# Kernel optimization log

Measured on AMD Instinct MI355X. Metric: run time of the kernel, lower is better.

## Reference

```python
import jax, jax.numpy as jnp
import numpy as np

K = 32  # num_nearest_neighbors

def silu(x):
    return x * jax.nn.sigmoid(x)

def setup_inputs() -> dict:
    key = jax.random.key(0)
    ks = jax.random.split(key, 10)
    b, n, d, m = 4, 2048, 64, 16
    e_in = 2 * d + 1  # 129 = fourier*2 + dim*2 + edge_dim + 1
    std = 0.001  # init_eps normal init on Linear weights
    inp = {
        "feats": jax.random.normal(ks[0], (b, n, d), dtype=jnp.float32),
        "coors": jax.random.normal(ks[1], (b, n, 3), dtype=jnp.float32),
        # edge_mlp: Linear(129,258) -> SiLU -> Linear(258,16) -> SiLU
        "ew1": jax.random.normal(ks[2], (e_in, 2 * e_in), dtype=jnp.float32) * std,
        "eb1": jnp.zeros((2 * e_in,), dtype=jnp.float32),
        "ew2": jax.random.normal(ks[3], (2 * e_in, m), dtype=jnp.float32) * std,
        "eb2": jnp.zeros((m,), dtype=jnp.float32),
        # coors_mlp: Linear(16,64) -> SiLU -> Linear(64,1)
        "cw1": jax.random.normal(ks[4], (m, 4 * m), dtype=jnp.float32) * std,
        "cb1": jnp.zeros((4 * m,), dtype=jnp.float32),
        "cw2": jax.random.normal(ks[5], (4 * m, 1), dtype=jnp.float32) * std,
        "cb2": jnp.zeros((1,), dtype=jnp.float32),
        # node_mlp: Linear(80,128) -> SiLU -> Linear(128,64)
        "nw1": jax.random.normal(ks[6], (d + m, 2 * d), dtype=jnp.float32) * std,
        "nb1": jnp.zeros((2 * d,), dtype=jnp.float32),
        "nw2": jax.random.normal(ks[7], (2 * d, d), dtype=jnp.float32) * std,
        "nb2": jnp.zeros((d,), dtype=jnp.float32),
    }
    return inp


def reference(feats, coors, ew1, eb1, ew2, eb2, cw1, cb1, cw2, cb2, nw1, nb1, nw2, nb2):
    b, n, d = feats.shape
    # pairwise relative coords / squared distances: [b,n,n,3], [b,n,n]
    rel = coors[:, :, None, :] - coors[:, None, :, :]
    dist2 = jnp.sum(rel * rel, axis=-1)
    # k nearest neighbors (smallest squared distance)
    _, idx = jax.lax.top_k(-dist2, K)  # idx: [b,n,K]
    bi = jnp.arange(b)[:, None, None]
    ii = jnp.arange(n)[None, :, None]
    rel_k = rel[bi, ii, idx]                # [b,n,K,3]
    dist_k = dist2[bi, ii, idx][..., None]  # [b,n,K,1]
    feats_j = feats[bi, idx]                # [b,n,K,d]
    feats_i = jnp.broadcast_to(feats[:, :, None, :], feats_j.shape)
    # edge MLP
    edge_in = jnp.concatenate([feats_i, feats_j, dist_k], axis=-1)  # [b,n,K,2d+1]
    h = silu(edge_in @ ew1 + eb1)
    m_ij = silu(h @ ew2 + eb2)  # [b,n,K,m]
    # coordinate update
    coor_w = (silu(m_ij @ cw1 + cb1) @ cw2 + cb2)[..., 0]  # [b,n,K]
    coors_out = jnp.einsum('bik,bikc->bic', coor_w, rel_k) + coors
    # node update (sum pooling over neighbors)
    m_i = jnp.sum(m_ij, axis=-2)  # [b,n,m]
    node_in = jnp.concatenate([feats, m_i], axis=-1)
    node_out = silu(node_in @ nw1 + nb1) @ nw2 + nb2 + feats
    return (node_out, coors_out)
```

## Files before the change

### kernel.cpp

```cpp
#include <hip/hip_runtime.h>
#include <math.h>

#define NB 4
#define NN 2048
#define ND 64
#define NM 16
#define NK 32
#define EIN 129
#define EH 258
#define CHD 64
#define NHD 128
#define PQS 288
#define KNN_BLOCKS (NB * NN / 4)
#define PREP_BLOCKS 90

typedef __attribute__((ext_vector_type(8))) short short8;
typedef __attribute__((ext_vector_type(4))) float f32x4;
typedef __attribute__((ext_vector_type(4))) int intx4;

__device__ __forceinline__ float fast_silu(float x) {
    return x * __builtin_amdgcn_rcpf(1.f + __expf(-x));
}

__device__ __forceinline__ short f2bf(float f) {
    union { float f; unsigned u; } v; v.f = f;
    unsigned r = v.u + 0x7FFFu + ((v.u >> 16) & 1u);
    return (short)(r >> 16);
}

__device__ __forceinline__ float bf2f(short s) {
    union { unsigned u; float f; } v;
    v.u = ((unsigned)(unsigned short)s) << 16;
    return v.f;
}

__device__ __forceinline__ unsigned cvt_pk_bf16(float lo, float hi) {
    unsigned r;
    asm("v_cvt_pk_bf16_f32 %0, %1, %2" : "=v"(r) : "v"(lo), "v"(hi));
    return r;
}

__device__ __forceinline__ unsigned umin_u(unsigned a, unsigned b) { return a < b ? a : b; }
__device__ __forceinline__ unsigned umax_u(unsigned a, unsigned b) { return a > b ? a : b; }

__global__ __launch_bounds__(256) void pk_kernel(
    const float* __restrict__ coors, int* __restrict__ idx_out,
    const float* __restrict__ ew1, const float* __restrict__ ew2, const float* __restrict__ eb1,
    const float* __restrict__ cw1,
    float* __restrict__ w1pad, float* __restrict__ eb1pad,
    short* __restrict__ W2T, short* __restrict__ W1F, short* __restrict__ cw1T) {
    __shared__ union {
        float clds[NN * 3];
        unsigned slds[4][NN];
    } sm;
    const int tid = threadIdx.x;

    if (blockIdx.x >= KNN_BLOCKS) {
        const int blk = blockIdx.x - KNN_BLOCKS;
        if (blk < 72) {
            const int kk = blk & 1, ct = (blk >> 1) % 18, half = blk / 36;
            for (int t = tid; t < 512; t += 256) {
                const int l = t >> 3, i = t & 7;
                const int er = l & 15, grp = l >> 4;
                const int k = kk * 32 + grp * 8 + i;
                const int col = ct * 16 + er;
                const int row = half * 64 + k;
                W1F[blk * 512 + t] = (col < EH) ? f2bf(ew1[row * EH + col]) : (short)0;
            }
        } else if (blk == 72) {
            for (int c = tid; c < PQS; c += 256) {
                w1pad[c] = (c < EH) ? ew1[128 * EH + c] : 0.f;
                eb1pad[c] = (c < EH) ? eb1[c] : 0.f;
            }
        } else if (blk < 89) {
            const int t = blk - 73;
            for (int k = tid; k < PQS; k += 256)
                W2T[t * PQS + k] = (k < EH) ? f2bf(ew2[k * NM + t]) : (short)0;
        } else {
            for (int t2 = tid; t2 < CHD * NM; t2 += 256) {
                const int h = t2 >> 4, t = t2 & 15;
                cw1T[t2] = f2bf(cw1[t * CHD + h]);
            }
        }
        return;
    }

    const int wv = tid >> 6;
    const int lane = tid & 63;
    const int row0 = blockIdx.x * 4;
    const int b = row0 >> 11;
    const float* cb = coors + (size_t)b * NN * 3;
    for (int t = tid; t < NN * 3; t += 256) sm.clds[t] = cb[t];
    __syncthreads();

    const int row = row0 + wv;
    const int i = row & (NN - 1);
    const float cix = sm.clds[i * 3 + 0], ciy = sm.clds[i * 3 + 1], ciz = sm.clds[i * 3 + 2];

    unsigned k[32];
    #pragma unroll
    for (int t = 0; t < 32; ++t) {
        int j = lane + 64 * t;
        float dx = cix - sm.clds[j * 3 + 0];
        float dy = ciy - sm.clds[j * 3 + 1];
        float dz = ciz - sm.clds[j * 3 + 2];
        float d = dx * dx + dy * dy + dz * dz;
        union { float f; unsigned u; } v; v.f = d;
        k[t] = (v.u & 0xFFFFF800u) | (unsigned)j;
    }
    __syncthreads();

    #pragma unroll
    for (int size = 2; size <= 32; size <<= 1) {
        #pragma unroll
        for (int stride = size >> 1; stride > 0; stride >>= 1) {
            #pragma unroll
            for (int t = 0; t < 32; ++t) {
                int p = t ^ stride;
                if (p > t) {
                    const bool up = ((t & size) == 0);
                    unsigned lo = umin_u(k[t], k[p]);
                    unsigned hi = umax_u(k[t], k[p]);
                    k[t] = up ? lo : hi;
                    k[p] = up ? hi : lo;
                }
            }
        }
    }
    #pragma unroll
    for (int t = 0; t < 32; ++t) sm.slds[wv][t * 64 + lane] = k[t];

    unsigned cur = k[0];
    int head = 0;
    int myidx = 0;
    for (int it = 0; it < NK; ++it) {
        unsigned w = cur;
        #pragma unroll
        for (int off = 1; off < 64; off <<= 1) {
            unsigned o = __shfl_xor(w, off);
            w = umin_u(w, o);
        }
        if (lane == it) myidx = (int)(w & 2047u);
        if (cur == w) {
            ++head;
            cur = (head < 32) ? sm.slds[wv][head * 64 + lane] : 0xFFFFFFFFu;
        }
    }
    if (lane < NK) idx_out[row * NK + lane] = myidx;
}

__global__ __launch_bounds__(256) void pq_kernel(const float* __restrict__ feats,
                                                 const short* __restrict__ W1F,
                                                 const float* __restrict__ eb1pad,
                                                 short* __restrict__ P,
                                                 short* __restrict__ Q) {
    const int wv = threadIdx.x >> 6, lane = threadIdx.x & 63;
    const int er = lane & 15, grp = lane >> 4;
    const int wid = blockIdx.x * 4 + wv;
    const int mt = wid / 18, ct = wid % 18;
    const int nb = mt * 16;

    short8 a[2];
    #pragma unroll
    for (int kk = 0; kk < 2; ++kk) {
        const float* fp = feats + (size_t)(nb + er) * ND + kk * 32 + grp * 8;
        f32x4 f0 = *(const f32x4*)fp;
        f32x4 f1 = *(const f32x4*)(fp + 4);
        union { intx4 iv; short8 s; } u;
        u.iv[0] = cvt_pk_bf16(f0[0], f0[1]);
        u.iv[1] = cvt_pk_bf16(f0[2], f0[3]);
        u.iv[2] = cvt_pk_bf16(f1[0], f1[1]);
        u.iv[3] = cvt_pk_bf16(f1[2], f1[3]);
        a[kk] = u.s;
    }

    const short8* WF = (const short8*)W1F;
    short8 bP0 = WF[((0 * 18 + ct) * 2 + 0) * 64 + lane];
    short8 bP1 = WF[((0 * 18 + ct) * 2 + 1) * 64 + lane];
    short8 bQ0 = WF[((1 * 18 + ct) * 2 + 0) * 64 + lane];
    short8 bQ1 = WF[((1 * 18 + ct) * 2 + 1) * 64 + lane];

    f32x4 accP = {0.f, 0.f, 0.f, 0.f};
    f32x4 accQ = {0.f, 0.f, 0.f, 0.f};
    accP = __builtin_amdgcn_mfma_f32_16x16x32_bf16(a[0], bP0, accP, 0, 0, 0);
    accP = __builtin_amdgcn_mfma_f32_16x16x32_bf16(a[1], bP1, accP, 0, 0, 0);
    accQ = __builtin_amdgcn_mfma_f32_16x16x32_bf16(a[0], bQ0, accQ, 0, 0, 0);
    accQ = __builtin_amdgcn_mfma_f32_16x16x32_bf16(a[1], bQ1, accQ, 0, 0, 0);

    const float bias = eb1pad[ct * 16 + er];
    #pragma unroll
    for (int r = 0; r < 4; ++r) {
        const int node = nb + grp * 4 + r;
        P[(size_t)node * PQS + ct * 16 + er] = f2bf(accP[r] + bias);
        Q[(size_t)node * PQS + ct * 16 + er] = f2bf(accQ[r]);
    }
}

__global__ __launch_bounds__(256) void edge_kernel(
    const float* __restrict__ coors, const int* __restrict__ idx,
    const short* __restrict__ P, const short* __restrict__ Q,
    const float* __restrict__ w1pad, const short* __restrict__ W2T,
    const float* __restrict__ eb2,
    const short* __restrict__ cw1T, const float* __restrict__ cb1,
    const float* __restrict__ cw2, const float* __restrict__ cb2,
    const float* __restrict__ feats,
    const float* __restrict__ nw1, const float* __restrict__ nb1,
    const float* __restrict__ nw2, const float* __restrict__ nb2,
    float* __restrict__ coors_out, float* __restrict__ node_out) {

    __shared__ __align__(16) short mtl[4][NK][NM];
    __shared__ float xs[4][80];
    __shared__ float hbuf[4][NHD];

    const int tid = threadIdx.x;
    const int wv = tid >> 6, lane = tid & 63;
    const int er = lane & 15, grp = lane >> 4;
    const int gi = blockIdx.x * 4 + wv;
    const int b = gi >> 11;

    xs[wv][lane] = feats[(size_t)gi * ND + lane];

    const int j0 = idx[gi * NK + er];
    const int j1 = idx[gi * NK + 16 + er];
    const float ci0 = coors[gi * 3 + 0], ci1 = coors[gi * 3 + 1], ci2 = coors[gi * 3 + 2];
    const float* cj0p = coors + (size_t)(b * NN + j0) * 3;
    const float* cj1p = coors + (size_t)(b * NN + j1) * 3;
    const float r0x = ci0 - cj0p[0], r0y = ci1 - cj0p[1], r0z = ci2 - cj0p[2];
    const float r1x = ci0 - cj1p[0], r1y = ci1 - cj1p[1], r1z = ci2 - cj1p[2];
    const float d0 = r0x * r0x + r0y * r0y + r0z * r0z;
    const float d1 = r1x * r1x + r1y * r1y + r1z * r1z;

    const short8* Pr8 = (const short8*)(P + (size_t)gi * PQS);
    const short8* Q0 = (const short8*)(Q + (size_t)(b * NN + j0) * PQS);
    const short8* Q1 = (const short8*)(Q + (size_t)(b * NN + j1) * PQS);
    const short8* w2row = (const short8*)(W2T + er * PQS);
    const f32x4* w14 = (const f32x4*)w1pad;

    f32x4 acc0 = {0.f, 0.f, 0.f, 0.f};
    f32x4 acc1 = {0.f, 0.f, 0.f, 0.f};
    #pragma unroll
    for (int kk = 0; kk < 9; ++kk) {
        short8 bf = w2row[kk * 4 + grp];
        short8 pb = Pr8[kk * 4 + grp];
        short8 qb0 = Q0[kk * 4 + grp];
        short8 qb1 = Q1[kk * 4 + grp];
        f32x4 w0 = w14[kk * 8 + grp * 2];
        f32x4 w1 = w14[kk * 8 + grp * 2 + 1];
        float wf[8] = {w0[0], w0[1], w0[2], w0[3], w1[0], w1[1], w1[2], w1[3]};
        float pf[8];
        #pragma unroll
        for (int i = 0; i < 8; ++i) pf[i] = bf2f(pb[i]);
        float h0[8], h1[8];
        #pragma unroll
        for (int i = 0; i < 8; ++i) {
            h0[i] = fast_silu(fmaf(d0, wf[i], pf[i]) + bf2f(qb0[i]));
            h1[i] = fast_silu(fmaf(d1, wf[i], pf[i]) + bf2f(qb1[i]));
        }
        union { intx4 iv; short8 s; } u0, u1;
        u0.iv[0] = cvt_pk_bf16(h0[0], h0[1]);
        u0.iv[1] = cvt_pk_bf16(h0[2], h0[3]);
        u0.iv[2] = cvt_pk_bf16(h0[4], h0[5]);
        u0.iv[3] = cvt_pk_bf16(h0[6], h0[7]);
        u1.iv[0] = cvt_pk_bf16(h1[0], h1[1]);
        u1.iv[1] = cvt_pk_bf16(h1[2], h1[3]);
        u1.iv[2] = cvt_pk_bf16(h1[4], h1[5]);
        u1.iv[3] = cvt_pk_bf16(h1[6], h1[7]);
        acc0 = __builtin_amdgcn_mfma_f32_16x16x32_bf16(u0.s, bf, acc0, 0, 0, 0);
        acc1 = __builtin_amdgcn_mfma_f32_16x16x32_bf16(u1.s, bf, acc1, 0, 0, 0);
    }

    const float eb2v = eb2[er];
    float m0[4], m1[4];
    #pragma unroll
    for (int r = 0; r < 4; ++r) {
        m0[r] = fast_silu(acc0[r] + eb2v);
        m1[r] = fast_silu(acc1[r] + eb2v);
    }

    float s = m0[0] + m0[1] + m0[2] + m0[3] + m1[0] + m1[1] + m1[2] + m1[3];
    s += __shfl_xor(s, 16);
    s += __shfl_xor(s, 32);
    if (lane < NM) xs[wv][ND + er] = s;

    #pragma unroll
    for (int r = 0; r < 4; ++r) {
        mtl[wv][grp * 4 + r][er] = f2bf(m0[r]);
        mtl[wv][16 + grp * 4 + r][er] = f2bf(m1[r]);
    }
    __syncthreads();

    const short8 zero8 = {0, 0, 0, 0, 0, 0, 0, 0};
    short8 afr[4];
    #pragma unroll
    for (int mt = 0; mt < 4; ++mt)
        afr[mt] = (grp < 2) ? *(const short8*)(cw1T + (mt * 16 + er) * NM + grp * 8) : zero8;

    float cwv[2];
    #pragma unroll
    for (int nt = 0; nt < 2; ++nt) {
        short8 bfr = (grp < 2) ? *(const short8*)&mtl[wv][nt * 16 + er][grp * 8] : zero8;
        float partial = 0.f;
        #pragma unroll
        for (int mt = 0; mt < 4; ++mt) {
            f32x4 dz = {0.f, 0.f, 0.f, 0.f};
            dz = __builtin_amdgcn_mfma_f32_16x16x32_bf16(afr[mt], bfr, dz, 0, 0, 0);
            f32x4 cb1v = *(const f32x4*)(cb1 + mt * 16 + grp * 4);
            f32x4 cw2v = *(const f32x4*)(cw2 + mt * 16 + grp * 4);
            #pragma unroll
            for (int r = 0; r < 4; ++r)
                partial += fast_silu(dz[r] + cb1v[r]) * cw2v[r];
        }
        partial += __shfl_xor(partial, 16);
        partial += __shfl_xor(partial, 32);
        cwv[nt] = partial + cb2[0];
    }

    float wx = cwv[0] * r0x + cwv[1] * r1x;
    float wy = cwv[0] * r0y + cwv[1] * r1y;
    float wz = cwv[0] * r0z + cwv[1] * r1z;
    #pragma unroll
    for (int off = 1; off < 16; off <<= 1) {
        wx += __shfl_xor(wx, off);
        wy += __shfl_xor(wy, off);
        wz += __shfl_xor(wz, off);
    }
    if (lane == 0) {
        coors_out[gi * 3 + 0] = ci0 + wx;
        coors_out[gi * 3 + 1] = ci1 + wy;
        coors_out[gi * 3 + 2] = ci2 + wz;
    }

    float a0 = nb1[lane], a1 = nb1[64 + lane];
    #pragma unroll 4
    for (int k = 0; k < 80; ++k) {
        float x = xs[wv][k];
        a0 += x * nw1[(size_t)k * NHD + lane];
        a1 += x * nw1[(size_t)k * NHD + 64 + lane];
    }
    hbuf[wv][lane] = fast_silu(a0);
    hbuf[wv][64 + lane] = fast_silu(a1);
    __syncthreads();

    float o = nb2[lane];
    #pragma unroll 4
    for (int k = 0; k < NHD; ++k) o += hbuf[wv][k] * nw2[(size_t)k * ND + lane];
    node_out[(size_t)gi * ND + lane] = o + xs[wv][lane];
}

extern "C" void kernel_launch(void* const* d_in, const int* in_sizes, int n_in,
                              void* d_out, int out_size, void* d_ws, size_t ws_size,
                              hipStream_t stream) {
    const float* feats = (const float*)d_in[0];
    const float* coors = (const float*)d_in[1];
    const float* ew1 = (const float*)d_in[2];
    const float* eb1 = (const float*)d_in[3];
    const float* ew2 = (const float*)d_in[4];
    const float* eb2 = (const float*)d_in[5];
    const float* cw1 = (const float*)d_in[6];
    const float* cb1 = (const float*)d_in[7];
    const float* cw2 = (const float*)d_in[8];
    const float* cb2 = (const float*)d_in[9];
    const float* nw1 = (const float*)d_in[10];
    const float* nb1 = (const float*)d_in[11];
    const float* nw2 = (const float*)d_in[12];
    const float* nb2 = (const float*)d_in[13];

    float* out_node = (float*)d_out;
    float* out_coors = out_node + (size_t)NB * NN * ND;

    char* ws = (char*)d_ws;
    int*   idx    = (int*)(ws + 0);
    short* P      = (short*)(ws + 1048576);
    short* Q      = (short*)(ws + 5767168);
    float* w1pad  = (float*)(ws + 10485760);
    float* eb1pad = (float*)(ws + 10486912);
    short* W2T    = (short*)(ws + 10488064);
    short* W1F    = (short*)(ws + 10497280);
    short* cw1T   = (short*)(ws + 10571008);

    pk_kernel<<<KNN_BLOCKS + PREP_BLOCKS, 256, 0, stream>>>(
        coors, idx, ew1, ew2, eb1, cw1, w1pad, eb1pad, W2T, W1F, cw1T);
    pq_kernel<<<(512 * 18) / 4, 256, 0, stream>>>(feats, W1F, eb1pad, P, Q);
    edge_kernel<<<NB * NN / 4, 256, 0, stream>>>(
        coors, idx, P, Q, w1pad, W2T, eb2, cw1T, cb1, cw2, cb2,
        feats, nw1, nb1, nw2, nb2, out_coors, out_node);
}
```

Before: 103.8 us.

## Move node MLP into separate MFMA kernel with bf16 staged inputs

Splits the node update out of the edge kernel into a new node_kernel that runs both node MLP layers with bf16 MFMA on 16-node tiles. Its input is staged through a bf16 global buffer: pq_kernel writes the feature part and edge_kernel writes the pooled messages. The node weights are pre-packed into MFMA fragment layout by extra prep blocks, and the hidden activations go through swizzled LDS. This replaces a per-wave scalar FP32 loop over 80x128 and 128x64 weights that re-read global memory. The cost is an extra launch and a global round trip, plus reduced precision on the node path, including rounding the message sums to bf16.

Measured after the change: 92.65 us. 10.8% less time.

```diff
diff --git a/kernel.cpp b/kernel.cpp
--- a/kernel.cpp
+++ b/kernel.cpp
@@ -11,8 +11,9 @@
 #define CHD 64
 #define NHD 128
 #define PQS 288
+#define XS 96
 #define KNN_BLOCKS (NB * NN / 4)
-#define PREP_BLOCKS 90
+#define PREP_BLOCKS 92
 
 typedef __attribute__((ext_vector_type(8))) short short8;
 typedef __attribute__((ext_vector_type(4))) float f32x4;
@@ -47,8 +48,10 @@
     const float* __restrict__ coors, int* __restrict__ idx_out,
     const float* __restrict__ ew1, const float* __restrict__ ew2, const float* __restrict__ eb1,
     const float* __restrict__ cw1,
+    const float* __restrict__ nw1, const float* __restrict__ nw2,
     float* __restrict__ w1pad, float* __restrict__ eb1pad,
-    short* __restrict__ W2T, short* __restrict__ W1F, short* __restrict__ cw1T) {
+    short* __restrict__ W2T, short* __restrict__ W1F, short* __restrict__ cw1T,
+    short* __restrict__ nw1F, short* __restrict__ nw2F) {
     __shared__ union {
         float clds[NN * 3];
         unsigned slds[4][NN];
@@ -76,10 +79,30 @@
             const int t = blk - 73;
             for (int k = tid; k < PQS; k += 256)
                 W2T[t * PQS + k] = (k < EH) ? f2bf(ew2[k * NM + t]) : (short)0;
-        } else {
+        } else if (blk == 89) {
             for (int t2 = tid; t2 < CHD * NM; t2 += 256) {
                 const int h = t2 >> 4, t = t2 & 15;
                 cw1T[t2] = f2bf(cw1[t * CHD + h]);
+            }
+        } else if (blk == 90) {
+            for (int t = tid; t < 24 * 512; t += 256) {
+                const int f = t >> 9, t2 = t & 511;
+                const int ct = f / 3, kk = f % 3;
+                const int l = t2 >> 3, i = t2 & 7;
+                const int er = l & 15, grp = l >> 4;
+                const int k = kk * 32 + grp * 8 + i;
+                const int col = ct * 16 + er;
+                nw1F[t] = (k < 80) ? f2bf(nw1[k * NHD + col]) : (short)0;
+            }
+        } else {
+            for (int t = tid; t < 16 * 512; t += 256) {
+                const int f = t >> 9, t2 = t & 511;
+                const int ct = f >> 2, kk = f & 3;
+                const int l = t2 >> 3, i = t2 & 7;
+                const int er = l & 15, grp = l >> 4;
+                const int k = kk * 32 + grp * 8 + i;
+                const int col = ct * 16 + er;
+                nw2F[t] = f2bf(nw2[k * ND + col]);
             }
         }
         return;
@@ -153,7 +176,8 @@
                                                  const short* __restrict__ W1F,
                                                  const float* __restrict__ eb1pad,
                                                  short* __restrict__ P,
-                                                 short* __restrict__ Q) {
+                                                 short* __restrict__ Q,
+                                                 short* __restrict__ xbuf) {
     const int wv = threadIdx.x >> 6, lane = threadIdx.x & 63;
     const int er = lane & 15, grp = lane >> 4;
     const int wid = blockIdx.x * 4 + wv;
@@ -174,6 +198,17 @@
         a[kk] = u.s;
     }
 
+    if (ct == 0) {
+        short* xr = xbuf + (size_t)(nb + er) * XS;
+        *(short8*)(xr + 0 * 32 + grp * 8) = a[0];
+        *(short8*)(xr + 1 * 32 + grp * 8) = a[1];
+        if (grp == 0) {
+            const short8 z8 = {0, 0, 0, 0, 0, 0, 0, 0};
+            *(short8*)(xr + 80) = z8;
+            *(short8*)(xr + 88) = z8;
+        }
+    }
+
     const short8* WF = (const short8*)W1F;
     short8 bP0 = WF[((0 * 18 + ct) * 2 + 0) * 64 + lane];
     short8 bP1 = WF[((0 * 18 + ct) * 2 + 1) * 64 + lane];
@@ -203,22 +238,15 @@
     const float* __restrict__ eb2,
     const short* __restrict__ cw1T, const float* __restrict__ cb1,
     const float* __restrict__ cw2, const float* __restrict__ cb2,
-    const float* __restrict__ feats,
-    const float* __restrict__ nw1, const float* __restrict__ nb1,
-    const float* __restrict__ nw2, const float* __restrict__ nb2,
-    float* __restrict__ coors_out, float* __restrict__ node_out) {
+    float* __restrict__ coors_out, short* __restrict__ xbuf) {
 
     __shared__ __align__(16) short mtl[4][NK][NM];
-    __shared__ float xs[4][80];
-    __shared__ float hbuf[4][NHD];
 
     const int tid = threadIdx.x;
     const int wv = tid >> 6, lane = tid & 63;
     const int er = lane & 15, grp = lane >> 4;
     const int gi = blockIdx.x * 4 + wv;
     const int b = gi >> 11;
-
-    xs[wv][lane] = feats[(size_t)gi * ND + lane];
 
     const int j0 = idx[gi * NK + er];
     const int j1 = idx[gi * NK + 16 + er];
@@ -280,7 +308,7 @@
     float s = m0[0] + m0[1] + m0[2] + m0[3] + m1[0] + m1[1] + m1[2] + m1[3];
     s += __shfl_xor(s, 16);
     s += __shfl_xor(s, 32);
-    if (lane < NM) xs[wv][ND + er] = s;
+    if (lane < NM) xbuf[(size_t)gi * XS + ND + er] = f2bf(s);
 
     #pragma unroll
     for (int r = 0; r < 4; ++r) {
@@ -329,22 +357,62 @@
         coors_out[gi * 3 + 1] = ci1 + wy;
         coors_out[gi * 3 + 2] = ci2 + wz;
     }
-
-    float a0 = nb1[lane], a1 = nb1[64 + lane];
-    #pragma unroll 4
-    for (int k = 0; k < 80; ++k) {
-        float x = xs[wv][k];
-        a0 += x * nw1[(size_t)k * NHD + lane];
-        a1 += x * nw1[(size_t)k * NHD + 64 + lane];
-    }
-    hbuf[wv][lane] = fast_silu(a0);
-    hbuf[wv][64 + lane] = fast_silu(a1);
+}
+
+__global__ __launch_bounds__(256) void node_kernel(
+    const short* __restrict__ xbuf,
+    const short* __restrict__ nw1F, const float* __restrict__ nb1,
+    const short* __restrict__ nw2F, const float* __restrict__ nb2,
+    const float* __restrict__ feats, float* __restrict__ node_out) {
+    __shared__ __align__(16) short hl[16 * 128];
+    const int tid = threadIdx.x;
+    const int wv = tid >> 6, lane = tid & 63;
+    const int er = lane & 15, grp = lane >> 4;
+    const int nb = blockIdx.x * 16;
+
+    short8 a[3];
+    #pragma unroll
+    for (int kk = 0; kk < 3; ++kk)
+        a[kk] = *(const short8*)(xbuf + (size_t)(nb + er) * XS + kk * 32 + grp * 8);
+
+    #pragma unroll
+    for (int c2 = 0; c2 < 2; ++c2) {
+        const int ct = wv * 2 + c2;
+        f32x4 acc = {0.f, 0.f, 0.f, 0.f};
+        #pragma unroll
+        for (int kk = 0; kk < 3; ++kk)
+            acc = __builtin_amdgcn_mfma_f32_16x16x32_bf16(
+                a[kk], *(const short8*)(nw1F + (ct * 3 + kk) * 512 + lane * 8), acc, 0, 0, 0);
+        const float b1 = nb1[ct * 16 + er];
+        #pragma unroll
+        for (int r = 0; r < 4; ++r) {
+            const int row = grp * 4 + r;
+            int byte = row * 256 + (ct * 16 + er) * 2;
+            byte ^= (row & 7) << 4;
+            *(short*)((char*)hl + byte) = f2bf(fast_silu(acc[r] + b1));
+        }
+    }
     __syncthreads();
 
-    float o = nb2[lane];
-    #pragma unroll 4
-    for (int k = 0; k < NHD; ++k) o += hbuf[wv][k] * nw2[(size_t)k * ND + lane];
-    node_out[(size_t)gi * ND + lane] = o + xs[wv][lane];
+    short8 a2[4];
+    #pragma unroll
+    for (int kk = 0; kk < 4; ++kk) {
+        int byte = er * 256 + kk * 64 + grp * 16;
+        byte ^= (er & 7) << 4;
+        a2[kk] = *(const short8*)((const char*)hl + byte);
+    }
+    f32x4 acc = {0.f, 0.f, 0.f, 0.f};
+    #pragma unroll
+    for (int kk = 0; kk < 4; ++kk)
+        acc = __builtin_amdgcn_mfma_f32_16x16x32_bf16(
+            a2[kk], *(const short8*)(nw2F + (wv * 4 + kk) * 512 + lane * 8), acc, 0, 0, 0);
+    const float b2 = nb2[wv * 16 + er];
+    #pragma unroll
+    for (int r = 0; r < 4; ++r) {
+        const int node = nb + grp * 4 + r;
+        node_out[(size_t)node * ND + wv * 16 + er] =
+            acc[r] + b2 + feats[(size_t)node * ND + wv * 16 + er];
+    }
 }
 
 extern "C" void kernel_launch(void* const* d_in, const int* in_sizes, int n_in,
@@ -377,11 +445,17 @@
     short* W2T    = (short*)(ws + 10488064);
     short* W1F    = (short*)(ws + 10497280);
     short* cw1T   = (short*)(ws + 10571008);
+    short* nw1F   = (short*)(ws + 10573056);
+    short* nw2F   = (short*)(ws + 10597632);
+    short* xbuf   = (short*)(ws + 10614016);
 
     pk_kernel<<<KNN_BLOCKS + PREP_BLOCKS, 256, 0, stream>>>(
-        coors, idx, ew1, ew2, eb1, cw1, w1pad, eb1pad, W2T, W1F, cw1T);
-    pq_kernel<<<(512 * 18) / 4, 256, 0, stream>>>(feats, W1F, eb1pad, P, Q);
+        coors, idx, ew1, ew2, eb1, cw1, nw1, nw2,
+        w1pad, eb1pad, W2T, W1F, cw1T, nw1F, nw2F);
+    pq_kernel<<<(512 * 18) / 4, 256, 0, stream>>>(feats, W1F, eb1pad, P, Q, xbuf);
     edge_kernel<<<NB * NN / 4, 256, 0, stream>>>(
         coors, idx, P, Q, w1pad, W2T, eb2, cw1T, cb1, cw2, cb2,
-        feats, nw1, nb1, nw2, nb2, out_coors, out_node);
-}
+        out_coors, xbuf);
+    node_kernel<<<NB * NN / 16, 256, 0, stream>>>(
+        xbuf, nw1F, nb1, nw2F, nb2, feats, out_node);
+}
```
